# Kernel tuning notes

Measured on AMD Instinct MI355X. Metric: run time of the kernel, lower is better.

Reference implementation:

```python
import jax, jax.numpy as jnp
import numpy as np

B, S, E = 2, 2048, 2048
H, HKV, D = 16, 8, 64          # num_heads, num_kv_heads, head_dim = E//H//2
NREP = H // HKV
DEPTH = 12
LAMBDA_INIT = 0.8 - 0.6 * float(np.exp(-0.3 * DEPTH))
EPS = 1e-5
SCALE = D ** -0.5
NEG = -1e30


def setup_inputs() -> dict:
    key = jax.random.key(0)
    ks = jax.random.split(key, 10)
    x = jax.random.normal(ks[0], (B, S, E), jnp.float32)
    # rotary tables (seq_len, head_dim/2)
    inv_freq = 1.0 / (10000.0 ** (np.arange(0, D, 2, dtype=np.float32) / D))
    freqs = jnp.asarray(np.outer(np.arange(S, dtype=np.float32), inv_freq), jnp.float32)
    cos, sin = jnp.cos(freqs), jnp.sin(freqs)
    Wq = jax.random.normal(ks[1], (E, E), jnp.float32) * 0.02
    Wk = jax.random.normal(ks[2], (E // NREP, E), jnp.float32) * 0.02
    Wv = jax.random.normal(ks[3], (E // NREP, E), jnp.float32) * 0.02
    Wo = jax.random.normal(ks[4], (E, E), jnp.float32) * 0.02
    lambda_q1 = jax.random.normal(ks[5], (D,), jnp.float32) * 0.1
    lambda_k1 = jax.random.normal(ks[6], (D,), jnp.float32) * 0.1
    lambda_q2 = jax.random.normal(ks[7], (D,), jnp.float32) * 0.1
    lambda_k2 = jax.random.normal(ks[8], (D,), jnp.float32) * 0.1
    subln_w = jnp.ones((2 * D,), jnp.float32)
    return dict(x=x, cos=cos, sin=sin, Wq=Wq, Wk=Wk, Wv=Wv, Wo=Wo,
                lambda_q1=lambda_q1, lambda_k1=lambda_k1,
                lambda_q2=lambda_q2, lambda_k2=lambda_k2, subln_w=subln_w)


def _rotary_interleaved(x, cos, sin):
    # x: (B, S, nh, D); cos/sin: (S, D//2); interleaved pairs (even, odd)
    x1, x2 = x[..., 0::2], x[..., 1::2]
    c = cos[None, :, None, :]
    s = sin[None, :, None, :]
    o1 = x1 * c - x2 * s
    o2 = x1 * s + x2 * c
    return jnp.stack([o1, o2], axis=-1).reshape(x.shape)


def _causal_attn(qh, kh, vcat, mask):
    # qh: (B,S,H,D); kh: (B,S,HKV,D); vcat: (B,S,HKV,2D)
    kr = jnp.repeat(kh, NREP, axis=2)      # GQA repeat -> (B,S,H,D)
    vr = jnp.repeat(vcat, NREP, axis=2)    # (B,S,H,2D)
    scores = jnp.einsum('bqhd,bkhd->bhqk', qh, kr) * SCALE
    scores = jnp.where(mask, scores, NEG)
    p = jax.nn.softmax(scores, axis=-1)
    return jnp.einsum('bhqk,bkhd->bqhd', p, vr)  # (B,S,H,2D)


def reference(x, cos, sin, Wq, Wk, Wv, Wo, lambda_q1, lambda_k1, lambda_q2, lambda_k2, subln_w):
    q = (x @ Wq.T).reshape(B, S, 2 * H, D)
    k = (x @ Wk.T).reshape(B, S, 2 * HKV, D)
    v = (x @ Wv.T).reshape(B, S, HKV, 2, D)
    q = _rotary_interleaved(q, cos, sin).reshape(B, S, H, 2, D)
    k = _rotary_interleaved(k, cos, sin).reshape(B, S, HKV, 2, D)
    vcat = v.reshape(B, S, HKV, 2 * D)  # concat(v1, v2) along last dim
    mask = jnp.tril(jnp.ones((S, S), bool))[None, None]
    a1 = _causal_attn(q[..., 0, :], k[..., 0, :], vcat, mask)
    a2 = _causal_attn(q[..., 1, :], k[..., 1, :], vcat, mask)
    lam = (jnp.exp(jnp.sum(lambda_q1 * lambda_k1))
           - jnp.exp(jnp.sum(lambda_q2 * lambda_k2)) + LAMBDA_INIT)
    a = a1 - lam * a2                      # (B,S,H,2D)
    # RMSNorm over last dim with affine weight, then fixed (1 - lambda_init) scale
    a = a * jax.lax.rsqrt(jnp.mean(a * a, axis=-1, keepdims=True) + EPS) * subln_w
    a = a * (1.0 - LAMBDA_INIT)
    return a.reshape(B, S, E) @ Wo.T
```

## Files before the change

### kernel.cpp

```cpp
#include <hip/hip_runtime.h>

#define LAMBDA_INIT 0.78360576653162448f

typedef __attribute__((ext_vector_type(8))) short short8;
typedef __attribute__((ext_vector_type(4))) float f32x4;

__device__ __forceinline__ unsigned short f2bf(float f) {
  unsigned int u; __builtin_memcpy(&u, &f, 4);
  u += 0x7fffu + ((u >> 16) & 1u);
  return (unsigned short)(u >> 16);
}
__device__ __forceinline__ short8 cvt8(float4 a, float4 b) {
  short8 s;
  s[0] = (short)f2bf(a.x); s[1] = (short)f2bf(a.y);
  s[2] = (short)f2bf(a.z); s[3] = (short)f2bf(a.w);
  s[4] = (short)f2bf(b.x); s[5] = (short)f2bf(b.y);
  s[6] = (short)f2bf(b.z); s[7] = (short)f2bf(b.w);
  return s;
}

#define GLOAD_LDS16(g, l)                                                     \
  __builtin_amdgcn_global_load_lds(                                           \
      (const __attribute__((address_space(1))) void*)(g),                     \
      (__attribute__((address_space(3))) void*)(l), 16, 0, 0)

__global__ void conv_bf16(const float* __restrict__ in,
                          unsigned short* __restrict__ outp, int n8) {
  const int i = blockIdx.x * 256 + threadIdx.x;
  if (i >= n8) return;
  const float4 a = *(const float4*)(in + (size_t)i * 8);
  const float4 b = *(const float4*)(in + (size_t)i * 8 + 4);
  *(short8*)(outp + (size_t)i * 8) = cvt8(a, b);
}

__global__ void conv_all(const float* __restrict__ x, const float* __restrict__ wq,
                         const float* __restrict__ wk, const float* __restrict__ wv,
                         const float* __restrict__ wo, unsigned short* __restrict__ ws) {
  const int i = blockIdx.x * 256 + threadIdx.x;
  const float* src; size_t so; unsigned short* dst;
  if (i < 1048576)      { src = x;  so = i;           dst = ws; }
  else if (i < 1572864) { src = wq; so = i - 1048576; dst = ws + 8388608; }
  else if (i < 1835008) { src = wk; so = i - 1572864; dst = ws + 12582912; }
  else if (i < 2097152) { src = wv; so = i - 1835008; dst = ws + 14680064; }
  else                  { src = wo; so = i - 2097152; dst = ws + 16777216; }
  const float4 a = *(const float4*)(src + so * 8);
  const float4 b = *(const float4*)(src + so * 8 + 4);
  *(short8*)(dst + so * 8) = cvt8(a, b);
}


__global__ __launch_bounds__(256, 2)
void qkv_bb(const unsigned short* __restrict__ xb,
            const unsigned short* __restrict__ Wqb, const unsigned short* __restrict__ Wkb,
            const unsigned short* __restrict__ Wvb, const float* __restrict__ cosb,
            const float* __restrict__ sinb,
            unsigned short* __restrict__ Qb, unsigned short* __restrict__ Kb,
            unsigned short* __restrict__ Vtb) {
  __shared__ __align__(16) unsigned short As[128 * 64];
  __shared__ __align__(16) unsigned short Bs[128 * 64];
  const int t = threadIdx.x;
  const int wave = t >> 6, lane = t & 63;
  const int l15 = lane & 15, l4 = lane >> 4;
  const int wm = (wave >> 1) * 64, wn = (wave & 1) * 64;
  const int m0 = blockIdx.y * 128, n0 = blockIdx.x * 128;
  const int crow = t >> 3, ccol = (t & 7) * 8;
  const unsigned short* Ag = xb + (size_t)m0 * 2048;

  const unsigned short* Bgh; int ntype;
  if (n0 < 2048)      { Bgh = Wqb + (size_t)n0 * 2048;          ntype = 0; }
  else if (n0 < 3072) { Bgh = Wkb + (size_t)(n0 - 2048) * 2048; ntype = 1; }
  else                { Bgh = Wvb + (size_t)(n0 - 3072) * 2048; ntype = 2; }

  const f32x4 fzero = {0.f, 0.f, 0.f, 0.f};
  f32x4 acc[4][4];
#pragma unroll
  for (int i = 0; i < 4; i++)
#pragma unroll
    for (int j = 0; j < 4; j++) acc[i][j] = fzero;

  for (int kt = 0; kt < 32; ++kt) {
    const int k0 = kt << 6;
    __syncthreads();
#pragma unroll
    for (int j = 0; j < 4; j++) {
      GLOAD_LDS16(Ag + (size_t)(j * 32 + crow) * 2048 + k0 + ccol,
                  &As[j * 2048 + wave * 512]);
      GLOAD_LDS16(Bgh + (size_t)(j * 32 + crow) * 2048 + k0 + ccol,
                  &Bs[j * 2048 + wave * 512]);
    }
    __syncthreads();
#pragma unroll
    for (int ks = 0; ks < 2; ++ks) {
      short8 af[4], bfr[4];
#pragma unroll
      for (int mi = 0; mi < 4; mi++)
        af[mi] = *(const short8*)(&As[(wm + mi * 16 + l15) * 64 + ks * 32 + l4 * 8]);
#pragma unroll
      for (int ni = 0; ni < 4; ni++)
        bfr[ni] = *(const short8*)(&Bs[(wn + ni * 16 + l15) * 64 + ks * 32 + l4 * 8]);
#pragma unroll
      for (int mi = 0; mi < 4; mi++)
#pragma unroll
        for (int ni = 0; ni < 4; ni++)
          acc[mi][ni] = __builtin_amdgcn_mfma_f32_16x16x32_bf16(af[mi], bfr[ni], acc[mi][ni], 0, 0, 0);
    }
  }
#pragma unroll
  for (int mi = 0; mi < 4; mi++)
#pragma unroll
    for (int ni = 0; ni < 4; ni++)
#pragma unroll
      for (int r = 0; r < 4; r++) {
        const int m = m0 + wm + mi * 16 + l4 * 4 + r;
        const int n = n0 + wn + ni * 16 + l15;
        float fv = acc[mi][ni][r];
        if (ntype < 2) {
          const int s = m & 2047;
          const int j = (n & 63) >> 1;
          const float c = cosb[s * 32 + j];
          const float sn = sinb[s * 32 + j];
          const float p = __shfl_xor(fv, 1);
          fv = (n & 1) ? (p * sn + fv * c) : (fv * c - p * sn);
        }
        if (ntype == 0)
          Qb[(size_t)m * 2048 + n] = f2bf(fv);
        else if (ntype == 1)
          Kb[(size_t)m * 1024 + (n - 2048)] = f2bf(fv);
        else
          Vtb[((size_t)((m >> 11) * 1024 + (n - 3072))) * 2048 + (m & 2047)] = f2bf(fv);
      }
}

__global__ __launch_bounds__(256, 2)
void o_bb(const unsigned short* __restrict__ Ab, const unsigned short* __restrict__ Wob,
          float* __restrict__ C) {
  __shared__ __align__(16) unsigned short As[128 * 64];
  __shared__ __align__(16) unsigned short Bs[128 * 64];
  const int t = threadIdx.x;
  const int wave = t >> 6, lane = t & 63;
  const int l15 = lane & 15, l4 = lane >> 4;
  const int wm = (wave >> 1) * 64, wn = (wave & 1) * 64;
  const int m0 = blockIdx.y * 128, n0 = blockIdx.x * 128;
  const int crow = t >> 3, ccol = (t & 7) * 8;
  const unsigned short* Ag = Ab + (size_t)m0 * 2048;
  const unsigned short* Bgh = Wob + (size_t)n0 * 2048;

  const f32x4 fzero = {0.f, 0.f, 0.f, 0.f};
  f32x4 acc[4][4];
#pragma unroll
  for (int i = 0; i < 4; i++)
#pragma unroll
    for (int j = 0; j < 4; j++) acc[i][j] = fzero;

  for (int kt = 0; kt < 32; ++kt) {
    const int k0 = kt << 6;
    __syncthreads();
#pragma unroll
    for (int j = 0; j < 4; j++) {
      GLOAD_LDS16(Ag + (size_t)(j * 32 + crow) * 2048 + k0 + ccol,
                  &As[j * 2048 + wave * 512]);
      GLOAD_LDS16(Bgh + (size_t)(j * 32 + crow) * 2048 + k0 + ccol,
                  &Bs[j * 2048 + wave * 512]);
    }
    __syncthreads();
#pragma unroll
    for (int ks = 0; ks < 2; ++ks) {
      short8 af[4], bfr[4];
#pragma unroll
      for (int mi = 0; mi < 4; mi++)
        af[mi] = *(const short8*)(&As[(wm + mi * 16 + l15) * 64 + ks * 32 + l4 * 8]);
#pragma unroll
      for (int ni = 0; ni < 4; ni++)
        bfr[ni] = *(const short8*)(&Bs[(wn + ni * 16 + l15) * 64 + ks * 32 + l4 * 8]);
#pragma unroll
      for (int mi = 0; mi < 4; mi++)
#pragma unroll
        for (int ni = 0; ni < 4; ni++)
          acc[mi][ni] = __builtin_amdgcn_mfma_f32_16x16x32_bf16(af[mi], bfr[ni], acc[mi][ni], 0, 0, 0);
    }
  }
#pragma unroll
  for (int mi = 0; mi < 4; mi++)
#pragma unroll
    for (int ni = 0; ni < 4; ni++)
#pragma unroll
      for (int r = 0; r < 4; r++) {
        const int m = m0 + wm + mi * 16 + l4 * 4 + r;
        const int n = n0 + wn + ni * 16 + l15;
        C[(size_t)m * 2048 + n] = acc[mi][ni][r];
      }
}


__global__ __launch_bounds__(256, 2)
void qkv_gemm_f32(const unsigned short* __restrict__ xb,
                  const float* __restrict__ Wq, const float* __restrict__ Wk,
                  const float* __restrict__ Wv, const float* __restrict__ cosb,
                  const float* __restrict__ sinb,
                  unsigned short* __restrict__ Qb, unsigned short* __restrict__ Kb,
                  unsigned short* __restrict__ Vtb) {
  __shared__ __align__(16) unsigned short As[128 * 64];
  __shared__ __align__(16) unsigned short Bs[128 * 72];
  const int t = threadIdx.x;
  const int wave = t >> 6, lane = t & 63;
  const int l15 = lane & 15, l4 = lane >> 4;
  const int wm = (wave >> 1) * 64, wn = (wave & 1) * 64;
  const int m0 = blockIdx.y * 128, n0 = blockIdx.x * 128;
  const int crow = t >> 3, ccol = (t & 7) * 8;
  const unsigned short* Ag = xb + (size_t)m0 * 2048;

  const float* Bg; int ntype;
  if (n0 < 2048)      { Bg = Wq + (size_t)n0 * 2048;          ntype = 0; }
  else if (n0 < 3072) { Bg = Wk + (size_t)(n0 - 2048) * 2048; ntype = 1; }
  else                { Bg = Wv + (size_t)(n0 - 3072) * 2048; ntype = 2; }

  const f32x4 fzero = {0.f, 0.f, 0.f, 0.f};
  f32x4 acc[4][4];
#pragma unroll
  for (int i = 0; i < 4; i++)
#pragma unroll
    for (int j = 0; j < 4; j++) acc[i][j] = fzero;

  float4 rbf[4][2];
#pragma unroll
  for (int i = 0; i < 4; i++) {
    rbf[i][0] = *(const float4*)(Bg + (size_t)(crow + 32 * i) * 2048 + ccol);
    rbf[i][1] = *(const float4*)(Bg + (size_t)(crow + 32 * i) * 2048 + ccol + 4);
  }
  for (int kt = 0; kt < 32; ++kt) {
    const int k0 = kt << 6;
    __syncthreads();
#pragma unroll
    for (int j = 0; j < 4; j++)
      GLOAD_LDS16(Ag + (size_t)(j * 32 + crow) * 2048 + k0 + ccol,
                  &As[j * 2048 + wave * 512]);
#pragma unroll
    for (int i = 0; i < 4; i++)
      *(short8*)(&Bs[(crow + 32 * i) * 72 + ccol]) = cvt8(rbf[i][0], rbf[i][1]);
    __syncthreads();
    if (kt + 1 < 32) {
      const int kn = k0 + 64;
#pragma unroll
      for (int i = 0; i < 4; i++) {
        rbf[i][0] = *(const float4*)(Bg + (size_t)(crow + 32 * i) * 2048 + kn + ccol);
        rbf[i][1] = *(const float4*)(Bg + (size_t)(crow + 32 * i) * 2048 + kn + ccol + 4);
      }
    }
#pragma unroll
    for (int ks = 0; ks < 2; ++ks) {
      short8 af[4], bfr[4];
#pragma unroll
      for (int mi = 0; mi < 4; mi++)
        af[mi] = *(const short8*)(&As[(wm + mi * 16 + l15) * 64 + ks * 32 + l4 * 8]);
#pragma unroll
      for (int ni = 0; ni < 4; ni++)
        bfr[ni] = *(const short8*)(&Bs[(wn + ni * 16 + l15) * 72 + ks * 32 + l4 * 8]);
#pragma unroll
      for (int mi = 0; mi < 4; mi++)
#pragma unroll
        for (int ni = 0; ni < 4; ni++)
          acc[mi][ni] = __builtin_amdgcn_mfma_f32_16x16x32_bf16(af[mi], bfr[ni], acc[mi][ni], 0, 0, 0);
    }
  }
#pragma unroll
  for (int mi = 0; mi < 4; mi++)
#pragma unroll
    for (int ni = 0; ni < 4; ni++)
#pragma unroll
      for (int r = 0; r < 4; r++) {
        const int m = m0 + wm + mi * 16 + l4 * 4 + r;
        const int n = n0 + wn + ni * 16 + l15;
        float fv = acc[mi][ni][r];
        if (ntype < 2) {
          const int s = m & 2047;
          const int j = (n & 63) >> 1;
          const float c = cosb[s * 32 + j];
          const float sn = sinb[s * 32 + j];
          const float p = __shfl_xor(fv, 1);
          fv = (n & 1) ? (p * sn + fv * c) : (fv * c - p * sn);
        }
        if (ntype == 0)
          Qb[(size_t)m * 2048 + n] = f2bf(fv);
        else if (ntype == 1)
          Kb[(size_t)m * 1024 + (n - 2048)] = f2bf(fv);
        else
          Vtb[((size_t)((m >> 11) * 1024 + (n - 3072))) * 2048 + (m & 2047)] = f2bf(fv);
      }
}

__global__ __launch_bounds__(256, 2)
void o_gemm_f32(const unsigned short* __restrict__ Ab, const float* __restrict__ Wo,
                float* __restrict__ C) {
  __shared__ __align__(16) unsigned short As[128 * 64];
  __shared__ __align__(16) unsigned short Bs[128 * 72];
  const int t = threadIdx.x;
  const int wave = t >> 6, lane = t & 63;
  const int l15 = lane & 15, l4 = lane >> 4;
  const int wm = (wave >> 1) * 64, wn = (wave & 1) * 64;
  const int m0 = blockIdx.y * 128, n0 = blockIdx.x * 128;
  const int crow = t >> 3, ccol = (t & 7) * 8;
  const unsigned short* Ag = Ab + (size_t)m0 * 2048;
  const float* Bg = Wo + (size_t)n0 * 2048;

  const f32x4 fzero = {0.f, 0.f, 0.f, 0.f};
  f32x4 acc[4][4];
#pragma unroll
  for (int i = 0; i < 4; i++)
#pragma unroll
    for (int j = 0; j < 4; j++) acc[i][j] = fzero;

  float4 rbf[4][2];
#pragma unroll
  for (int i = 0; i < 4; i++) {
    rbf[i][0] = *(const float4*)(Bg + (size_t)(crow + 32 * i) * 2048 + ccol);
    rbf[i][1] = *(const float4*)(Bg + (size_t)(crow + 32 * i) * 2048 + ccol + 4);
  }
  for (int kt = 0; kt < 32; ++kt) {
    const int k0 = kt << 6;
    __syncthreads();
#pragma unroll
    for (int j = 0; j < 4; j++)
      GLOAD_LDS16(Ag + (size_t)(j * 32 + crow) * 2048 + k0 + ccol,
                  &As[j * 2048 + wave * 512]);
#pragma unroll
    for (int i = 0; i < 4; i++)
      *(short8*)(&Bs[(crow + 32 * i) * 72 + ccol]) = cvt8(rbf[i][0], rbf[i][1]);
    __syncthreads();
    if (kt + 1 < 32) {
      const int kn = k0 + 64;
#pragma unroll
      for (int i = 0; i < 4; i++) {
        rbf[i][0] = *(const float4*)(Bg + (size_t)(crow + 32 * i) * 2048 + kn + ccol);
        rbf[i][1] = *(const float4*)(Bg + (size_t)(crow + 32 * i) * 2048 + kn + ccol + 4);
      }
    }
#pragma unroll
    for (int ks = 0; ks < 2; ++ks) {
      short8 af[4], bfr[4];
#pragma unroll
      for (int mi = 0; mi < 4; mi++)
        af[mi] = *(const short8*)(&As[(wm + mi * 16 + l15) * 64 + ks * 32 + l4 * 8]);
#pragma unroll
      for (int ni = 0; ni < 4; ni++)
        bfr[ni] = *(const short8*)(&Bs[(wn + ni * 16 + l15) * 72 + ks * 32 + l4 * 8]);
#pragma unroll
      for (int mi = 0; mi < 4; mi++)
#pragma unroll
        for (int ni = 0; ni < 4; ni++)
          acc[mi][ni] = __builtin_amdgcn_mfma_f32_16x16x32_bf16(af[mi], bfr[ni], acc[mi][ni], 0, 0, 0);
    }
  }
#pragma unroll
  for (int mi = 0; mi < 4; mi++)
#pragma unroll
    for (int ni = 0; ni < 4; ni++)
#pragma unroll
      for (int r = 0; r < 4; r++) {
        const int m = m0 + wm + mi * 16 + l4 * 4 + r;
        const int n = n0 + wn + ni * 16 + l15;
        C[(size_t)m * 2048 + n] = acc[mi][ni][r];
      }
}

__global__ __launch_bounds__(256, 2)
void attn_kernel(const unsigned short* __restrict__ Q,
                 const unsigned short* __restrict__ Kb,
                 const unsigned short* __restrict__ Vt,
                 unsigned short* __restrict__ Ab,
                 const float* __restrict__ lq1,
                 const float* __restrict__ lk1,
                 const float* __restrict__ lq2,
                 const float* __restrict__ lk2,
                 const float* __restrict__ wsub) {
  const int pi = blockIdx.x;
  const int bh = blockIdx.y;
  const int b = bh >> 4, h = bh & 15, hk = h >> 1;
  __shared__ __align__(16) unsigned short Ks[2][64 * 72];
  __shared__ __align__(16) unsigned short Vs[128 * 72];
  __shared__ __align__(16) unsigned short Ps[2][64 * 72];
  const int t = threadIdx.x;
  const int wave = t >> 6, lane = t & 63;
  const int l15 = lane & 15, l4 = lane >> 4;
  const int crow = t >> 3, ccol = (t & 7) * 8;

  float s1 = 0.f, s2 = 0.f;
  for (int i = 0; i < 64; i++) {
    s1 += lq1[i] * lk1[i];
    s2 += lq2[i] * lk2[i];
  }
  const float lam = __expf(s1) - __expf(s2) + LAMBDA_INIT;

  float wv[8];
#pragma unroll
  for (int nt = 0; nt < 8; nt++) wv[nt] = wsub[nt * 16 + l15];

  short8 onesf;
#pragma unroll
  for (int j = 0; j < 8; j++) onesf[j] = (l15 == 0) ? (short)0x3F80 : (short)0;

  const f32x4 fzero = {0.f, 0.f, 0.f, 0.f};
  const unsigned short* Kgb = Kb + ((size_t)(b * 2048)) * 1024 + 2 * hk * 64;
  const unsigned short* Vgb = Vt + ((size_t)((b * 8 + hk) * 128)) * 2048;

  for (int half = 0; half < 2; ++half) {
    const int qi = half ? (31 - pi) : pi;
    const int q0 = qi * 64;

    __syncthreads();
#pragma unroll
    for (int c = 0; c < 2; c++) {
      const unsigned short* Qg = Q + ((size_t)(b * 2048 + q0)) * 2048 + (2 * h + c) * 64;
#pragma unroll
      for (int i = 0; i < 2; i++) {
        const int row = crow + 32 * i;
        *(int4*)(&Ps[c][row * 72 + ccol]) = *(const int4*)(Qg + (size_t)row * 2048 + ccol);
      }
    }
    __syncthreads();
    short8 qf[2][2];
#pragma unroll
    for (int c = 0; c < 2; c++)
#pragma unroll
      for (int ks = 0; ks < 2; ks++)
        qf[c][ks] = *(const short8*)(&Ps[c][(wave * 16 + l15) * 72 + ks * 32 + l4 * 8]);

    f32x4 accO[2][8], accL[2];
#pragma unroll
    for (int c = 0; c < 2; c++) {
      accL[c] = fzero;
#pragma unroll
      for (int nt = 0; nt < 8; nt++) accO[c][nt] = fzero;
    }

    int4 rk[2][2], rv[4];
#pragma unroll
    for (int c = 0; c < 2; c++)
#pragma unroll
      for (int i = 0; i < 2; i++)
        rk[c][i] = *(const int4*)(Kgb + (size_t)(crow + 32 * i) * 1024 + c * 64 + ccol);
#pragma unroll
    for (int i = 0; i < 4; i++)
      rv[i] = *(const int4*)(Vgb + (size_t)(crow + 32 * i) * 2048 + ccol);

    for (int kt = 0; kt <= qi; ++kt) {
      const int k0 = kt * 64;
      __syncthreads();
#pragma unroll
      for (int c = 0; c < 2; c++)
#pragma unroll
        for (int i = 0; i < 2; i++)
          *(int4*)(&Ks[c][(crow + 32 * i) * 72 + ccol]) = rk[c][i];
#pragma unroll
      for (int i = 0; i < 4; i++)
        *(int4*)(&Vs[(crow + 32 * i) * 72 + ccol]) = rv[i];
      __syncthreads();
      if (kt < qi) {
        const int kn = k0 + 64;
#pragma unroll
        for (int c = 0; c < 2; c++)
#pragma unroll
          for (int i = 0; i < 2; i++)
            rk[c][i] = *(const int4*)(Kgb + (size_t)(kn + crow + 32 * i) * 1024 + c * 64 + ccol);
#pragma unroll
        for (int i = 0; i < 4; i++)
          rv[i] = *(const int4*)(Vgb + (size_t)(crow + 32 * i) * 2048 + kn + ccol);
      }
      const bool diag = (kt == qi);
#pragma unroll
      for (int c = 0; c < 2; c++) {
        f32x4 sc[4];
#pragma unroll
        for (int ct = 0; ct < 4; ct++) {
          const short8 kb0 = *(const short8*)(&Ks[c][(ct * 16 + l15) * 72 + 0 + l4 * 8]);
          const short8 kb1 = *(const short8*)(&Ks[c][(ct * 16 + l15) * 72 + 32 + l4 * 8]);
          f32x4 z = fzero;
          z = __builtin_amdgcn_mfma_f32_16x16x32_bf16(qf[c][0], kb0, z, 0, 0, 0);
          z = __builtin_amdgcn_mfma_f32_16x16x32_bf16(qf[c][1], kb1, z, 0, 0, 0);
          sc[ct] = z;
        }
#pragma unroll
        for (int r = 0; r < 4; r++) {
          const int qrow = q0 + wave * 16 + l4 * 4 + r;
#pragma unroll
          for (int ct = 0; ct < 4; ct++) {
            float e = __expf(fmaf(sc[ct][r], 0.125f, -16.0f));
            if (diag && (k0 + ct * 16 + l15) > qrow) e = 0.f;
            Ps[c][(wave * 16 + l4 * 4 + r) * 72 + ct * 16 + l15] = f2bf(e);
          }
        }
      }
      short8 pf[2][2];
#pragma unroll
      for (int c = 0; c < 2; c++)
#pragma unroll
        for (int ks = 0; ks < 2; ks++)
          pf[c][ks] = *(const short8*)(&Ps[c][(wave * 16 + l15) * 72 + ks * 32 + l4 * 8]);
#pragma unroll
      for (int nt = 0; nt < 8; nt++) {
        const short8 v0 = *(const short8*)(&Vs[(nt * 16 + l15) * 72 + 0 + l4 * 8]);
        const short8 v1 = *(const short8*)(&Vs[(nt * 16 + l15) * 72 + 32 + l4 * 8]);
        accO[0][nt] = __builtin_amdgcn_mfma_f32_16x16x32_bf16(pf[0][0], v0, accO[0][nt], 0, 0, 0);
        accO[0][nt] = __builtin_amdgcn_mfma_f32_16x16x32_bf16(pf[0][1], v1, accO[0][nt], 0, 0, 0);
        accO[1][nt] = __builtin_amdgcn_mfma_f32_16x16x32_bf16(pf[1][0], v0, accO[1][nt], 0, 0, 0);
        accO[1][nt] = __builtin_amdgcn_mfma_f32_16x16x32_bf16(pf[1][1], v1, accO[1][nt], 0, 0, 0);
      }
      accL[0] = __builtin_amdgcn_mfma_f32_16x16x32_bf16(pf[0][0], onesf, accL[0], 0, 0, 0);
      accL[0] = __builtin_amdgcn_mfma_f32_16x16x32_bf16(pf[0][1], onesf, accL[0], 0, 0, 0);
      accL[1] = __builtin_amdgcn_mfma_f32_16x16x32_bf16(pf[1][0], onesf, accL[1], 0, 0, 0);
      accL[1] = __builtin_amdgcn_mfma_f32_16x16x32_bf16(pf[1][1], onesf, accL[1], 0, 0, 0);
    }

#pragma unroll
    for (int r = 0; r < 4; r++) {
      const float l1 = __shfl(accL[0][r], lane & 48);
      const float l2 = __shfl(accL[1][r], lane & 48);
      const float i1 = 1.f / fmaxf(l1, 1e-30f);
      const float i2 = lam / fmaxf(l2, 1e-30f);
      float av[8], ss = 0.f;
#pragma unroll
      for (int nt = 0; nt < 8; nt++) {
        const float a = accO[0][nt][r] * i1 - accO[1][nt][r] * i2;
        av[nt] = a;
        ss += a * a;
      }
#pragma unroll
      for (int off = 1; off < 16; off <<= 1) ss += __shfl_xor(ss, off, 16);
      const float sca = rsqrtf(ss * (1.f / 128.f) + 1e-5f) * (1.f - LAMBDA_INIT);
      const int qrow = q0 + wave * 16 + l4 * 4 + r;
      unsigned short* Ao = Ab + ((size_t)(b * 2048 + qrow)) * 2048 + h * 128;
#pragma unroll
      for (int nt = 0; nt < 8; nt++)
        Ao[nt * 16 + l15] = f2bf(av[nt] * sca * wv[nt]);
    }
  }
}

extern "C" void kernel_launch(void* const* d_in, const int* in_sizes, int n_in,
                              void* d_out, int out_size, void* d_ws, size_t ws_size,
                              hipStream_t stream) {
  const float* x    = (const float*)d_in[0];
  const float* cosb = (const float*)d_in[1];
  const float* sinb = (const float*)d_in[2];
  const float* Wq   = (const float*)d_in[3];
  const float* Wk   = (const float*)d_in[4];
  const float* Wv   = (const float*)d_in[5];
  const float* Wo   = (const float*)d_in[6];
  const float* lq1  = (const float*)d_in[7];
  const float* lk1  = (const float*)d_in[8];
  const float* lq2  = (const float*)d_in[9];
  const float* lk2  = (const float*)d_in[10];
  const float* wsub = (const float*)d_in[11];
  float* out = (float*)d_out;

  unsigned short* XA  = (unsigned short*)d_ws;
  unsigned short* Kb  = (unsigned short*)d_out;
  unsigned short* Vtb = Kb + (size_t)4096 * 1024;
  unsigned short* Qb  = Vtb + (size_t)2 * 1024 * 2048;

  dim3 blk(256);
  if (ws_size >= (size_t)41943040) {
    unsigned short* Wqb = XA + 8388608;
    unsigned short* Wkb = XA + 12582912;
    unsigned short* Wvb = XA + 14680064;
    unsigned short* Wob = XA + 16777216;
    conv_all<<<10240, blk, 0, stream>>>(x, Wq, Wk, Wv, Wo, XA);
    qkv_bb<<<dim3(32, 32), blk, 0, stream>>>(XA, Wqb, Wkb, Wvb, cosb, sinb, Qb, Kb, Vtb);
    attn_kernel<<<dim3(16, 32), blk, 0, stream>>>(Qb, Kb, Vtb, XA, lq1, lk1, lq2, lk2, wsub);
    o_bb<<<dim3(16, 32), blk, 0, stream>>>(XA, Wob, out);
  } else {
    conv_bf16<<<4096, blk, 0, stream>>>(x, XA, 1048576);
    qkv_gemm_f32<<<dim3(32, 32), blk, 0, stream>>>(XA, Wq, Wk, Wv, cosb, sinb, Qb, Kb, Vtb);
    attn_kernel<<<dim3(16, 32), blk, 0, stream>>>(Qb, Kb, Vtb, XA, lq1, lk1, lq2, lk2, wsub);
    o_gemm_f32<<<dim3(16, 32), blk, 0, stream>>>(XA, Wo, out);
  }
}
```

Baseline: 430.5 us.

## Enlarge attention query tile to 128 rows with swizzled direct-to-LDS loads

Measured after the change: 446.3 us. 3.7% more time.

```diff
diff --git a/kernel.cpp b/kernel.cpp
--- a/kernel.cpp
+++ b/kernel.cpp
@@ -375,13 +375,19 @@
   const int pi = blockIdx.x;
   const int bh = blockIdx.y;
   const int b = bh >> 4, h = bh & 15, hk = h >> 1;
-  __shared__ __align__(16) unsigned short Ks[2][64 * 72];
-  __shared__ __align__(16) unsigned short Vs[128 * 72];
-  __shared__ __align__(16) unsigned short Ps[2][64 * 72];
+  const int qi = b ? (15 - pi) : pi;
+  const int q0 = qi * 128;
+  const int nkt = 2 * qi + 2;
+
+  __shared__ __align__(16) unsigned short Ks[2][64 * 64];
+  __shared__ __align__(16) unsigned short Vs[128 * 64];
+  __shared__ __align__(16) unsigned short Ps[128 * 64];
+
   const int t = threadIdx.x;
   const int wave = t >> 6, lane = t & 63;
   const int l15 = lane & 15, l4 = lane >> 4;
   const int crow = t >> 3, ccol = (t & 7) * 8;
+  const int swc = ccol ^ ((crow & 7) << 3);
 
   float s1 = 0.f, s2 = 0.f;
   for (int i = 0; i < 64; i++) {
@@ -390,149 +396,138 @@
   }
   const float lam = __expf(s1) - __expf(s2) + LAMBDA_INIT;
 
-  float wv[8];
-#pragma unroll
-  for (int nt = 0; nt < 8; nt++) wv[nt] = wsub[nt * 16 + l15];
-
   short8 onesf;
 #pragma unroll
   for (int j = 0; j < 8; j++) onesf[j] = (l15 == 0) ? (short)0x3F80 : (short)0;
 
+  const int wrow = q0 + wave * 32;
+  short8 qf[2][2][2];
+#pragma unroll
+  for (int s = 0; s < 2; s++)
+#pragma unroll
+    for (int c = 0; c < 2; c++)
+#pragma unroll
+      for (int ks = 0; ks < 2; ks++)
+        qf[s][c][ks] = *(const short8*)(Q + ((size_t)(b * 2048 + wrow + s * 16 + l15)) * 2048
+                                          + (2 * h + c) * 64 + ks * 32 + l4 * 8);
+
   const f32x4 fzero = {0.f, 0.f, 0.f, 0.f};
+  f32x4 accO[2][2][8];
+  f32x4 accL[2][2];
+#pragma unroll
+  for (int s = 0; s < 2; s++)
+#pragma unroll
+    for (int c = 0; c < 2; c++) {
+      accL[s][c] = fzero;
+#pragma unroll
+      for (int nt = 0; nt < 8; nt++) accO[s][c][nt] = fzero;
+    }
+
   const unsigned short* Kgb = Kb + ((size_t)(b * 2048)) * 1024 + 2 * hk * 64;
   const unsigned short* Vgb = Vt + ((size_t)((b * 8 + hk) * 128)) * 2048;
 
-  for (int half = 0; half < 2; ++half) {
-    const int qi = half ? (31 - pi) : pi;
-    const int q0 = qi * 64;
-
-    __syncthreads();
+  for (int kt = 0; kt < nkt; ++kt) {
+    const int k0 = kt << 6;
+    __syncthreads();
+#pragma unroll
+    for (int c = 0; c < 2; c++)
+#pragma unroll
+      for (int i = 0; i < 2; i++)
+        GLOAD_LDS16(Kgb + (size_t)(k0 + i * 32 + crow) * 1024 + c * 64 + swc,
+                    &Ks[c][i * 2048 + wave * 512]);
+#pragma unroll
+    for (int i = 0; i < 4; i++)
+      GLOAD_LDS16(Vgb + (size_t)(i * 32 + crow) * 2048 + k0 + swc,
+                  &Vs[i * 2048 + wave * 512]);
+    __syncthreads();
+
+    short8 pf[2][2][2];
 #pragma unroll
     for (int c = 0; c < 2; c++) {
-      const unsigned short* Qg = Q + ((size_t)(b * 2048 + q0)) * 2048 + (2 * h + c) * 64;
-#pragma unroll
-      for (int i = 0; i < 2; i++) {
-        const int row = crow + 32 * i;
-        *(int4*)(&Ps[c][row * 72 + ccol]) = *(const int4*)(Qg + (size_t)row * 2048 + ccol);
-      }
-    }
-    __syncthreads();
-    short8 qf[2][2];
-#pragma unroll
-    for (int c = 0; c < 2; c++)
-#pragma unroll
-      for (int ks = 0; ks < 2; ks++)
-        qf[c][ks] = *(const short8*)(&Ps[c][(wave * 16 + l15) * 72 + ks * 32 + l4 * 8]);
-
-    f32x4 accO[2][8], accL[2];
-#pragma unroll
-    for (int c = 0; c < 2; c++) {
-      accL[c] = fzero;
-#pragma unroll
-      for (int nt = 0; nt < 8; nt++) accO[c][nt] = fzero;
-    }
-
-    int4 rk[2][2], rv[4];
-#pragma unroll
-    for (int c = 0; c < 2; c++)
-#pragma unroll
-      for (int i = 0; i < 2; i++)
-        rk[c][i] = *(const int4*)(Kgb + (size_t)(crow + 32 * i) * 1024 + c * 64 + ccol);
-#pragma unroll
-    for (int i = 0; i < 4; i++)
-      rv[i] = *(const int4*)(Vgb + (size_t)(crow + 32 * i) * 2048 + ccol);
-
-    for (int kt = 0; kt <= qi; ++kt) {
-      const int k0 = kt * 64;
-      __syncthreads();
-#pragma unroll
-      for (int c = 0; c < 2; c++)
-#pragma unroll
-        for (int i = 0; i < 2; i++)
-          *(int4*)(&Ks[c][(crow + 32 * i) * 72 + ccol]) = rk[c][i];
-#pragma unroll
-      for (int i = 0; i < 4; i++)
-        *(int4*)(&Vs[(crow + 32 * i) * 72 + ccol]) = rv[i];
-      __syncthreads();
-      if (kt < qi) {
-        const int kn = k0 + 64;
-#pragma unroll
-        for (int c = 0; c < 2; c++)
-#pragma unroll
-          for (int i = 0; i < 2; i++)
-            rk[c][i] = *(const int4*)(Kgb + (size_t)(kn + crow + 32 * i) * 1024 + c * 64 + ccol);
-#pragma unroll
-        for (int i = 0; i < 4; i++)
-          rv[i] = *(const int4*)(Vgb + (size_t)(crow + 32 * i) * 2048 + kn + ccol);
-      }
-      const bool diag = (kt == qi);
-#pragma unroll
-      for (int c = 0; c < 2; c++) {
-        f32x4 sc[4];
-#pragma unroll
-        for (int ct = 0; ct < 4; ct++) {
-          const short8 kb0 = *(const short8*)(&Ks[c][(ct * 16 + l15) * 72 + 0 + l4 * 8]);
-          const short8 kb1 = *(const short8*)(&Ks[c][(ct * 16 + l15) * 72 + 32 + l4 * 8]);
+#pragma unroll
+      for (int ct = 0; ct < 4; ct++) {
+        const int kr = ct * 16 + l15;
+        const int ksw = (kr & 7) << 3;
+        const short8 kb0 = *(const short8*)(&Ks[c][kr * 64 + ((l4 * 8) ^ ksw)]);
+        const short8 kb1 = *(const short8*)(&Ks[c][kr * 64 + ((32 + l4 * 8) ^ ksw)]);
+#pragma unroll
+        for (int s = 0; s < 2; s++) {
           f32x4 z = fzero;
-          z = __builtin_amdgcn_mfma_f32_16x16x32_bf16(qf[c][0], kb0, z, 0, 0, 0);
-          z = __builtin_amdgcn_mfma_f32_16x16x32_bf16(qf[c][1], kb1, z, 0, 0, 0);
-          sc[ct] = z;
-        }
-#pragma unroll
-        for (int r = 0; r < 4; r++) {
-          const int qrow = q0 + wave * 16 + l4 * 4 + r;
-#pragma unroll
-          for (int ct = 0; ct < 4; ct++) {
-            float e = __expf(fmaf(sc[ct][r], 0.125f, -16.0f));
-            if (diag && (k0 + ct * 16 + l15) > qrow) e = 0.f;
-            Ps[c][(wave * 16 + l4 * 4 + r) * 72 + ct * 16 + l15] = f2bf(e);
+          z = __builtin_amdgcn_mfma_f32_16x16x32_bf16(qf[s][c][0], kb0, z, 0, 0, 0);
+          z = __builtin_amdgcn_mfma_f32_16x16x32_bf16(qf[s][c][1], kb1, z, 0, 0, 0);
+          const int rbase = wave * 32 + s * 16 + l4 * 4;
+          const bool needm = (k0 + 63) > (q0 + wave * 32 + s * 16);
+#pragma unroll
+          for (int r = 0; r < 4; r++) {
+            float e = exp2f(fmaf(z[r], 0.18033688011112042f, -23.083120654223414f));
+            if (needm && (k0 + ct * 16 + l15) > (q0 + rbase + r)) e = 0.f;
+            const int prow = rbase + r;
+            Ps[prow * 64 + ((ct * 16 + l15) ^ ((prow & 7) << 3))] = f2bf(e);
           }
         }
       }
-      short8 pf[2][2];
-#pragma unroll
-      for (int c = 0; c < 2; c++)
+#pragma unroll
+      for (int s = 0; s < 2; s++) {
+        const int prow = wave * 32 + s * 16 + l15;
+        const int psw = (l15 & 7) << 3;
 #pragma unroll
         for (int ks = 0; ks < 2; ks++)
-          pf[c][ks] = *(const short8*)(&Ps[c][(wave * 16 + l15) * 72 + ks * 32 + l4 * 8]);
-#pragma unroll
-      for (int nt = 0; nt < 8; nt++) {
-        const short8 v0 = *(const short8*)(&Vs[(nt * 16 + l15) * 72 + 0 + l4 * 8]);
-        const short8 v1 = *(const short8*)(&Vs[(nt * 16 + l15) * 72 + 32 + l4 * 8]);
-        accO[0][nt] = __builtin_amdgcn_mfma_f32_16x16x32_bf16(pf[0][0], v0, accO[0][nt], 0, 0, 0);
-        accO[0][nt] = __builtin_amdgcn_mfma_f32_16x16x32_bf16(pf[0][1], v1, accO[0][nt], 0, 0, 0);
-        accO[1][nt] = __builtin_amdgcn_mfma_f32_16x16x32_bf16(pf[1][0], v0, accO[1][nt], 0, 0, 0);
-        accO[1][nt] = __builtin_amdgcn_mfma_f32_16x16x32_bf16(pf[1][1], v1, accO[1][nt], 0, 0, 0);
-      }
-      accL[0] = __builtin_amdgcn_mfma_f32_16x16x32_bf16(pf[0][0], onesf, accL[0], 0, 0, 0);
-      accL[0] = __builtin_amdgcn_mfma_f32_16x16x32_bf16(pf[0][1], onesf, accL[0], 0, 0, 0);
-      accL[1] = __builtin_amdgcn_mfma_f32_16x16x32_bf16(pf[1][0], onesf, accL[1], 0, 0, 0);
-      accL[1] = __builtin_amdgcn_mfma_f32_16x16x32_bf16(pf[1][1], onesf, accL[1], 0, 0, 0);
-    }
-
+          pf[s][c][ks] = *(const short8*)(&Ps[prow * 64 + ((ks * 32 + l4 * 8) ^ psw)]);
+      }
+    }
+
+    __builtin_amdgcn_s_setprio(1);
+#pragma unroll
+    for (int nt = 0; nt < 8; nt++) {
+      const int vrow = nt * 16 + l15;
+      const int vsw = (vrow & 7) << 3;
+      const short8 v0 = *(const short8*)(&Vs[vrow * 64 + ((l4 * 8) ^ vsw)]);
+      const short8 v1 = *(const short8*)(&Vs[vrow * 64 + ((32 + l4 * 8) ^ vsw)]);
+#pragma unroll
+      for (int s = 0; s < 2; s++) {
+        accO[s][0][nt] = __builtin_amdgcn_mfma_f32_16x16x32_bf16(pf[s][0][0], v0, accO[s][0][nt], 0, 0, 0);
+        accO[s][0][nt] = __builtin_amdgcn_mfma_f32_16x16x32_bf16(pf[s][0][1], v1, accO[s][0][nt], 0, 0, 0);
+        accO[s][1][nt] = __builtin_amdgcn_mfma_f32_16x16x32_bf16(pf[s][1][0], v0, accO[s][1][nt], 0, 0, 0);
+        accO[s][1][nt] = __builtin_amdgcn_mfma_f32_16x16x32_bf16(pf[s][1][1], v1, accO[s][1][nt], 0, 0, 0);
+      }
+    }
+#pragma unroll
+    for (int s = 0; s < 2; s++)
+#pragma unroll
+      for (int c = 0; c < 2; c++) {
+        accL[s][c] = __builtin_amdgcn_mfma_f32_16x16x32_bf16(pf[s][c][0], onesf, accL[s][c], 0, 0, 0);
+        accL[s][c] = __builtin_amdgcn_mfma_f32_16x16x32_bf16(pf[s][c][1], onesf, accL[s][c], 0, 0, 0);
+      }
+    __builtin_amdgcn_s_setprio(0);
+  }
+
+  float wv[8];
+#pragma unroll
+  for (int nt = 0; nt < 8; nt++) wv[nt] = wsub[nt * 16 + l15];
+#pragma unroll
+  for (int s = 0; s < 2; s++)
 #pragma unroll
     for (int r = 0; r < 4; r++) {
-      const float l1 = __shfl(accL[0][r], lane & 48);
-      const float l2 = __shfl(accL[1][r], lane & 48);
+      const float l1 = __shfl(accL[s][0][r], lane & 48);
+      const float l2 = __shfl(accL[s][1][r], lane & 48);
       const float i1 = 1.f / fmaxf(l1, 1e-30f);
       const float i2 = lam / fmaxf(l2, 1e-30f);
       float av[8], ss = 0.f;
 #pragma unroll
       for (int nt = 0; nt < 8; nt++) {
-        const float a = accO[0][nt][r] * i1 - accO[1][nt][r] * i2;
+        const float a = accO[s][0][nt][r] * i1 - accO[s][1][nt][r] * i2;
         av[nt] = a;
         ss += a * a;
       }
 #pragma unroll
       for (int off = 1; off < 16; off <<= 1) ss += __shfl_xor(ss, off, 16);
       const float sca = rsqrtf(ss * (1.f / 128.f) + 1e-5f) * (1.f - LAMBDA_INIT);
-      const int qrow = q0 + wave * 16 + l4 * 4 + r;
+      const int qrow = q0 + wave * 32 + s * 16 + l4 * 4 + r;
       unsigned short* Ao = Ab + ((size_t)(b * 2048 + qrow)) * 2048 + h * 128;
 #pragma unroll
       for (int nt = 0; nt < 8; nt++)
         Ao[nt * 16 + l15] = f2bf(av[nt] * sca * wv[nt]);
     }
-  }
 }
 
 extern "C" void kernel_launch(void* const* d_in, const int* in_sizes, int n_in,
```
